# Kernel tuning notes

Measured on AMD Instinct MI355X. Metric: run time of the kernel, lower is better.

The kernel has to match this reference:

```python
import jax, jax.numpy as jnp
import numpy as np

KS = 3
STRIDE = 2

def _parabolic_kernel(t, ks):
    # z_i = linspace(-ks//2 + 1, ks//2, ks)  (python floor-div semantics)
    lo = (-ks) // 2 + 1
    hi = ks // 2
    z_i = jnp.linspace(float(lo), float(hi), ks, dtype=jnp.float32)
    z = z_i[:, None] ** 2 + z_i[None, :] ** 2          # (ks, ks)
    z = z / z[0, 0]                                     # normalize by corner value
    return -z[None, :, :] * t[:, None, None]            # (C, ks, ks)

def _maxplus_pool(f, h, ks, stride):
    # out[b,c,i,j] = max_{p,q} f[b,c,i*s+p, j*s+q] + h[c,p,q]  (valid padding)
    B, C, H, W = f.shape
    oH = (H - ks) // stride + 1
    oW = (W - ks) // stride + 1
    out = None
    for p in range(ks):
        for q in range(ks):
            win = f[:, :, p:p + (oH - 1) * stride + 1:stride,
                          q:q + (oW - 1) * stride + 1:stride]
            v = win + h[None, :, p, q, None, None]
            out = v if out is None else jnp.maximum(out, v)
    return out

def setup_inputs() -> dict:
    key = jax.random.key(0)
    kf, kt = jax.random.split(key)
    f = jax.random.normal(kf, (16, 256, 128, 128), dtype=jnp.float32)
    t = jax.random.normal(kt, (256,), dtype=jnp.float32)  # per-channel parabola scale
    return {"f": f, "t": t}

def reference(f, t):
    h = _parabolic_kernel(t, KS)        # (C, ks, ks)
    return _maxplus_pool(f, h, KS, STRIDE)
```

## Files before the change

kernel.cpp:

```cpp
#include <hip/hip_runtime.h>


#define C_DIM 256
#define H_DIM 128
#define W_DIM 128
#define OH 63
#define OW 63

__global__ __launch_bounds__(256) void parab_pool_kernel(
    const float* __restrict__ f,
    const float* __restrict__ t,
    float* __restrict__ out,
    int total)
{
    int idx = blockIdx.x * blockDim.x + threadIdx.x;
    if (idx >= total) return;

    int j   = idx % OW;
    int tmp = idx / OW;
    int i   = tmp % OH;
    int bc  = tmp / OH;
    int c   = bc % C_DIM;

    const float a = -t[c];

    const float* base = f + ((bc * H_DIM + 2 * i) * W_DIM + 2 * j);

    float r00 = base[0];
    float r01 = base[1];
    float r02 = base[2];
    float r10 = base[W_DIM + 0];
    float r11 = base[W_DIM + 1];
    float r12 = base[W_DIM + 2];
    float r20 = base[2 * W_DIM + 0];
    float r21 = base[2 * W_DIM + 1];
    float r22 = base[2 * W_DIM + 2];

    float corners = fmaxf(fmaxf(r00, r02), fmaxf(r20, r22));
    float edges   = fmaxf(fmaxf(r01, r10), fmaxf(r12, r21));

    float v = fmaxf(r11, fmaxf(corners + a, edges + 0.5f * a));
    out[idx] = v;
}

extern "C" void kernel_launch(void* const* d_in, const int* in_sizes, int n_in,
                              void* d_out, int out_size, void* d_ws, size_t ws_size,
                              hipStream_t stream)
{
    const float* f = (const float*)d_in[0];
    const float* t = (const float*)d_in[1];
    float* out = (float*)d_out;

    int total = out_size;
    int block = 256;
    int grid = (total + block - 1) / block;

    parab_pool_kernel<<<grid, block, 0, stream>>>(f, t, out, total);
}
```

Before: 61.75 us.

## Compute four outputs per thread with vectorized float4 row loads

Measured after the change: 67.14 us. 1.09x slower.

```diff
diff --git a/kernel.cpp b/kernel.cpp
--- a/kernel.cpp
+++ b/kernel.cpp
@@ -6,41 +6,67 @@
 #define W_DIM 128
 #define OH 63
 #define OW 63
+#define ROWS_TOTAL (16 * C_DIM * OH)
 
-__global__ __launch_bounds__(256) void parab_pool_kernel(
+__global__ __launch_bounds__(256) void parab_pool_v2(
     const float* __restrict__ f,
     const float* __restrict__ t,
-    float* __restrict__ out,
-    int total)
+    float* __restrict__ out)
 {
-    int idx = blockIdx.x * blockDim.x + threadIdx.x;
-    if (idx >= total) return;
+    int tid = blockIdx.x * blockDim.x + threadIdx.x;
+    int k   = tid & 15;
+    int row = tid >> 4;
 
-    int j   = idx % OW;
-    int tmp = idx / OW;
-    int i   = tmp % OH;
-    int bc  = tmp / OH;
-    int c   = bc % C_DIM;
+    int i  = row % OH;
+    int bc = row / OH;
+    int c  = bc & (C_DIM - 1);
 
-    const float a = -t[c];
+    const float a  = -t[c];
+    const float ha = 0.5f * a;
 
-    const float* base = f + ((bc * H_DIM + 2 * i) * W_DIM + 2 * j);
+    const bool full = (k != 15);
 
-    float r00 = base[0];
-    float r01 = base[1];
-    float r02 = base[2];
-    float r10 = base[W_DIM + 0];
-    float r11 = base[W_DIM + 1];
-    float r12 = base[W_DIM + 2];
-    float r20 = base[2 * W_DIM + 0];
-    float r21 = base[2 * W_DIM + 1];
-    float r22 = base[2 * W_DIM + 2];
+    const float* base = f + ((size_t)(bc * H_DIM + 2 * i)) * W_DIM + 8 * k;
 
-    float corners = fmaxf(fmaxf(r00, r02), fmaxf(r20, r22));
-    float edges   = fmaxf(fmaxf(r01, r10), fmaxf(r12, r21));
+    float r0[9], r1[9], r2[9];
+    {
+        float4 A = *(const float4*)(base);
+        float4 B = *(const float4*)(base + 4);
+        r0[0]=A.x; r0[1]=A.y; r0[2]=A.z; r0[3]=A.w;
+        r0[4]=B.x; r0[5]=B.y; r0[6]=B.z; r0[7]=B.w;
+        r0[8] = full ? base[8] : 0.0f;
+    }
+    {
+        const float* p = base + W_DIM;
+        float4 A = *(const float4*)(p);
+        float4 B = *(const float4*)(p + 4);
+        r1[0]=A.x; r1[1]=A.y; r1[2]=A.z; r1[3]=A.w;
+        r1[4]=B.x; r1[5]=B.y; r1[6]=B.z; r1[7]=B.w;
+        r1[8] = full ? p[8] : 0.0f;
+    }
+    {
+        const float* p = base + 2 * W_DIM;
+        float4 A = *(const float4*)(p);
+        float4 B = *(const float4*)(p + 4);
+        r2[0]=A.x; r2[1]=A.y; r2[2]=A.z; r2[3]=A.w;
+        r2[4]=B.x; r2[5]=B.y; r2[6]=B.z; r2[7]=B.w;
+        r2[8] = full ? p[8] : 0.0f;
+    }
 
-    float v = fmaxf(r11, fmaxf(corners + a, edges + 0.5f * a));
-    out[idx] = v;
+    float res[4];
+    #pragma unroll
+    for (int l = 0; l < 4; ++l) {
+        const int c0 = 2 * l, c1 = 2 * l + 1, c2 = 2 * l + 2;
+        float corners = fmaxf(fmaxf(r0[c0], r0[c2]), fmaxf(r2[c0], r2[c2]));
+        float edges   = fmaxf(fmaxf(r0[c1], r2[c1]), fmaxf(r1[c0], r1[c2]));
+        res[l] = fmaxf(r1[c1], fmaxf(corners + a, edges + ha));
+    }
+
+    float* o = out + (size_t)row * OW + 4 * k;
+    o[0] = res[0];
+    o[1] = res[1];
+    o[2] = res[2];
+    if (full) o[3] = res[3];
 }
 
 extern "C" void kernel_launch(void* const* d_in, const int* in_sizes, int n_in,
@@ -51,9 +77,9 @@
     const float* t = (const float*)d_in[1];
     float* out = (float*)d_out;
 
-    int total = out_size;
+    int total_threads = ROWS_TOTAL * 16;
     int block = 256;
-    int grid = (total + block - 1) / block;
+    int grid = total_threads / block;
 
-    parab_pool_kernel<<<grid, block, 0, stream>>>(f, t, out, total);
+    parab_pool_v2<<<grid, block, 0, stream>>>(f, t, out);
 }
```

## Compute 4x9 output tile per thread with float4 row loads and row reuse

Applied to the files above, without the earlier changes.

Result: slower. 80.74 us (+30.7%).

```diff
diff --git a/kernel.cpp b/kernel.cpp
--- a/kernel.cpp
+++ b/kernel.cpp
@@ -6,41 +6,65 @@
 #define W_DIM 128
 #define OH 63
 #define OW 63
+#define SEGS 7
+#define RPS 9
 
-__global__ __launch_bounds__(256) void parab_pool_kernel(
+__global__ __launch_bounds__(256) void parab_pool_v3(
     const float* __restrict__ f,
     const float* __restrict__ t,
-    float* __restrict__ out,
-    int total)
+    float* __restrict__ out)
 {
-    int idx = blockIdx.x * blockDim.x + threadIdx.x;
-    if (idx >= total) return;
+    int tid  = blockIdx.x * blockDim.x + threadIdx.x;
+    int k    = tid & 15;
+    int rest = tid >> 4;
+    int s    = rest % SEGS;
+    int bc   = rest / SEGS;
+    int c    = bc & (C_DIM - 1);
 
-    int j   = idx % OW;
-    int tmp = idx / OW;
-    int i   = tmp % OH;
-    int bc  = tmp / OH;
-    int c   = bc % C_DIM;
+    const float a  = -t[c];
+    const float ha = 0.5f * a;
+    const bool full = (k != 15);
+    const int  tail = full ? 8 : 0;
 
-    const float a = -t[c];
+    const float* base = f + ((size_t)(bc * H_DIM + 18 * s)) * W_DIM + 8 * k;
+    float* ob = out + ((size_t)(bc * OH + RPS * s)) * OW + 4 * k;
 
-    const float* base = f + ((bc * H_DIM + 2 * i) * W_DIM + 2 * j);
+    float top[9], mid[9], bot[9];
 
-    float r00 = base[0];
-    float r01 = base[1];
-    float r02 = base[2];
-    float r10 = base[W_DIM + 0];
-    float r11 = base[W_DIM + 1];
-    float r12 = base[W_DIM + 2];
-    float r20 = base[2 * W_DIM + 0];
-    float r21 = base[2 * W_DIM + 1];
-    float r22 = base[2 * W_DIM + 2];
+#define LOAD_ROW(dst, P) do { \
+    const float* _p = (P); \
+    float4 _A = *(const float4*)(_p); \
+    float4 _B = *(const float4*)(_p + 4); \
+    dst[0]=_A.x; dst[1]=_A.y; dst[2]=_A.z; dst[3]=_A.w; \
+    dst[4]=_B.x; dst[5]=_B.y; dst[6]=_B.z; dst[7]=_B.w; \
+    dst[8]=_p[tail]; } while (0)
 
-    float corners = fmaxf(fmaxf(r00, r02), fmaxf(r20, r22));
-    float edges   = fmaxf(fmaxf(r01, r10), fmaxf(r12, r21));
+    LOAD_ROW(top, base);
 
-    float v = fmaxf(r11, fmaxf(corners + a, edges + 0.5f * a));
-    out[idx] = v;
+    #pragma unroll
+    for (int it = 0; it < RPS; ++it) {
+        LOAD_ROW(mid, base + (2 * it + 1) * W_DIM);
+        LOAD_ROW(bot, base + (2 * it + 2) * W_DIM);
+
+        float res[4];
+        #pragma unroll
+        for (int l = 0; l < 4; ++l) {
+            const int c0 = 2 * l, c1 = 2 * l + 1, c2 = 2 * l + 2;
+            float corners = fmaxf(fmaxf(top[c0], top[c2]), fmaxf(bot[c0], bot[c2]));
+            float edges   = fmaxf(fmaxf(top[c1], bot[c1]), fmaxf(mid[c0], mid[c2]));
+            res[l] = fmaxf(mid[c1], fmaxf(corners + a, edges + ha));
+        }
+
+        float* o = ob + it * OW;
+        __builtin_nontemporal_store(res[0], o + 0);
+        __builtin_nontemporal_store(res[1], o + 1);
+        __builtin_nontemporal_store(res[2], o + 2);
+        if (full) __builtin_nontemporal_store(res[3], o + 3);
+
+        #pragma unroll
+        for (int x = 0; x < 9; ++x) top[x] = bot[x];
+    }
+#undef LOAD_ROW
 }
 
 extern "C" void kernel_launch(void* const* d_in, const int* in_sizes, int n_in,
@@ -51,9 +75,9 @@
     const float* t = (const float*)d_in[1];
     float* out = (float*)d_out;
 
-    int total = out_size;
+    int total_threads = 16 * C_DIM * SEGS * 16;
     int block = 256;
-    int grid = (total + block - 1) / block;
+    int grid = total_threads / block;
 
-    parab_pool_kernel<<<grid, block, 0, stream>>>(f, t, out, total);
+    parab_pool_v3<<<grid, block, 0, stream>>>(f, t, out);
 }
```
